# Kernel tuning notes

Hardware: AMD Instinct MI355X
Metric: run time of the kernel (lower is better)

The kernel has to match this reference:

```python
import jax, jax.numpy as jnp
import numpy as np

B, N, M = 1024, 65536, 128


def setup_inputs() -> dict:
    key = jax.random.key(0)
    k1, k2, k3, k4 = jax.random.split(key, 4)
    address = jax.random.uniform(k1, (B, N), dtype=jnp.float32)
    erase = jax.random.uniform(k2, (B, M), dtype=jnp.float32)
    add = jax.random.normal(k3, (B, M), dtype=jnp.float32)
    content = jax.random.uniform(k4, (N, M), dtype=jnp.float32)
    return {"address": address, "erase": erase, "add": add, "content": content}


def reference(address, erase, add, content):
    # write: outer-product erase/add aggregated over batch -> [N, M]
    erase_v = jnp.einsum('bn,bm->nm', address, erase)
    add_v = jnp.einsum('bn,bm->nm', address, add)
    new_content = content * (1.0 - erase_v) + add_v
    # read-after-write: [B,N] @ [N,M] -> [B,M]
    read_content = jnp.einsum('bn,nm->bm', address, new_content)
    return read_content
```

## Files before the change

kernel.cpp:

```cpp
#include <hip/hip_runtime.h>
#include <hip/hip_bf16.h>
#include <stdint.h>

#define B_SZ 1024
#define N_SZ 65536
#define M_SZ 128

typedef short bf16x8 __attribute__((ext_vector_type(8)));
typedef short bf16x4 __attribute__((ext_vector_type(4)));
typedef float f32x4 __attribute__((ext_vector_type(4)));

__device__ __forceinline__ unsigned short f2bf(float f) {
    uint32_t u = __float_as_uint(f);
    uint32_t r = (u + 0x7FFFu + ((u >> 16) & 1u)) >> 16;
    return (unsigned short)r;
}

__global__ __launch_bounds__(256) void k_edt(const float* __restrict__ E,
                                             const float* __restrict__ D,
                                             unsigned short* __restrict__ EDt) {
    __shared__ float tile[32][33];
    int bx = blockIdx.x & 31;
    int cy = blockIdx.x >> 5;
    int b0 = bx * 32, c0 = cy * 32;
    const float* src = (c0 < M_SZ) ? E : D;
    int cs0 = c0 & (M_SZ - 1);
    int t = threadIdx.x;
    int i = t >> 3, j = (t & 7) * 4;
    const float* p = src + (size_t)(b0 + i) * M_SZ + cs0 + j;
    float4 v = *(const float4*)p;
    tile[i][j] = v.x; tile[i][j + 1] = v.y; tile[i][j + 2] = v.z; tile[i][j + 3] = v.w;
    __syncthreads();
    int c = t >> 3, b4 = (t & 7) * 4;
    unsigned short* q = EDt + (size_t)(c0 + c) * B_SZ + b0 + b4;
    ushort4 o;
    o.x = f2bf(tile[b4 + 0][c]); o.y = f2bf(tile[b4 + 1][c]);
    o.z = f2bf(tile[b4 + 2][c]); o.w = f2bf(tile[b4 + 3][c]);
    *(ushort4*)q = o;
}

__global__ __launch_bounds__(256) void k_zero(float* __restrict__ out) {
    int i = blockIdx.x * 1024 + threadIdx.x * 4;
    *(float4*)(out + i) = (float4){0.f, 0.f, 0.f, 0.f};
}

#define AS_LD 132
#define ED_LD 40

__global__ __launch_bounds__(256, 2) void k_pass1(
    const float* __restrict__ A,
    const unsigned short* __restrict__ EDt,
    const float* __restrict__ C,
    unsigned short* __restrict__ NCt)
{
    __shared__ __align__(16) unsigned short As[2][32 * AS_LD];
    __shared__ __align__(16) unsigned short EDs[2][256 * ED_LD];
    const int t = threadIdx.x;
    const int lane = t & 63;
    const int wv = t >> 6;
    const int wvn = wv >> 1, wvc = wv & 1;
    const int g = lane >> 4;
    const int m16 = lane & 15;
    const int n0 = blockIdx.x * 128;

    const int kb = t >> 3;
    const int cA = (t & 7) * 16;
    const int colq = t >> 3;
    const int seg = t & 7;

    int cb[8];
#pragma unroll
    for (int fj = 0; fj < 4; ++fj) { cb[fj] = wvc * 4 + fj; cb[fj + 4] = 8 + wvc * 4 + fj; }

    f32x4 acc[4][8];
#pragma unroll
    for (int i = 0; i < 4; ++i)
#pragma unroll
        for (int j = 0; j < 8; ++j) acc[i][j] = (f32x4){0.f, 0.f, 0.f, 0.f};

    {
        const float* p = A + (size_t)kb * N_SZ + n0 + cA;
        float4 a0 = ((const float4*)p)[0], a1 = ((const float4*)p)[1];
        float4 a2 = ((const float4*)p)[2], a3 = ((const float4*)p)[3];
        ushort4* w = (ushort4*)&As[0][kb * AS_LD + cA];
        ushort4 o;
        o.x = f2bf(a0.x); o.y = f2bf(a0.y); o.z = f2bf(a0.z); o.w = f2bf(a0.w); w[0] = o;
        o.x = f2bf(a1.x); o.y = f2bf(a1.y); o.z = f2bf(a1.z); o.w = f2bf(a1.w); w[1] = o;
        o.x = f2bf(a2.x); o.y = f2bf(a2.y); o.z = f2bf(a2.z); o.w = f2bf(a2.w); w[2] = o;
        o.x = f2bf(a3.x); o.y = f2bf(a3.y); o.z = f2bf(a3.z); o.w = f2bf(a3.w); w[3] = o;
#pragma unroll
        for (int p8 = 0; p8 < 8; ++p8) {
            int col = p8 * 32 + colq;
            ushort4 v = *(const ushort4*)(EDt + (size_t)col * B_SZ + seg * 4);
            *(ushort4*)&EDs[0][col * ED_LD + seg * 4] = v;
        }
    }
    __syncthreads();

    int cur = 0;
    for (int bk = 0; bk < B_SZ; bk += 32) {
        const bool last = (bk + 32 >= B_SZ);
        const int nk = last ? 0 : bk + 32;

        const float* p = A + (size_t)(nk + kb) * N_SZ + n0 + cA;
        float4 a0 = ((const float4*)p)[0], a1 = ((const float4*)p)[1];
        float4 a2 = ((const float4*)p)[2], a3 = ((const float4*)p)[3];
        ushort4 e[8];
#pragma unroll
        for (int p8 = 0; p8 < 8; ++p8) {
            int col = p8 * 32 + colq;
            e[p8] = *(const ushort4*)(EDt + (size_t)col * B_SZ + nk + seg * 4);
        }

        bf16x8 af[4];
#pragma unroll
        for (int fi = 0; fi < 4; ++fi) {
            int nl = wvn * 64 + fi * 16 + m16;
#pragma unroll
            for (int j = 0; j < 8; ++j)
                af[fi][j] = (short)As[cur][(g * 8 + j) * AS_LD + nl];
        }
        bf16x8 bfr[8];
#pragma unroll
        for (int fj = 0; fj < 8; ++fj)
            bfr[fj] = *(const bf16x8*)&EDs[cur][(cb[fj] * 16 + m16) * ED_LD + g * 8];

#pragma unroll
        for (int fj = 0; fj < 8; ++fj)
#pragma unroll
            for (int fi = 0; fi < 4; ++fi)
                acc[fi][fj] = __builtin_amdgcn_mfma_f32_16x16x32_bf16(af[fi], bfr[fj], acc[fi][fj], 0, 0, 0);

        if (!last) {
            const int nxt = cur ^ 1;
            ushort4* w = (ushort4*)&As[nxt][kb * AS_LD + cA];
            ushort4 o;
            o.x = f2bf(a0.x); o.y = f2bf(a0.y); o.z = f2bf(a0.z); o.w = f2bf(a0.w); w[0] = o;
            o.x = f2bf(a1.x); o.y = f2bf(a1.y); o.z = f2bf(a1.z); o.w = f2bf(a1.w); w[1] = o;
            o.x = f2bf(a2.x); o.y = f2bf(a2.y); o.z = f2bf(a2.z); o.w = f2bf(a2.w); w[2] = o;
            o.x = f2bf(a3.x); o.y = f2bf(a3.y); o.z = f2bf(a3.z); o.w = f2bf(a3.w); w[3] = o;
#pragma unroll
            for (int p8 = 0; p8 < 8; ++p8) {
                int col = p8 * 32 + colq;
                *(ushort4*)&EDs[nxt][col * ED_LD + seg * 4] = e[p8];
            }
        }
        __syncthreads();
        cur ^= 1;
    }

#pragma unroll
    for (int fi = 0; fi < 4; ++fi)
#pragma unroll
        for (int fj = 0; fj < 4; ++fj) {
            int n_base = n0 + wvn * 64 + fi * 16 + g * 4;
            int m = wvc * 64 + fj * 16 + m16;
            bf16x4 o;
#pragma unroll
            for (int r = 0; r < 4; ++r) {
                float w = acc[fi][fj][r];
                float v = acc[fi][fj + 4][r];
                float cc = C[(size_t)(n_base + r) * M_SZ + m];
                o[r] = (short)f2bf(cc * (1.0f - w) + v);
            }
            *(bf16x4*)&NCt[(size_t)m * N_SZ + n_base] = o;
        }
}

#define L2_LD 40

__global__ __launch_bounds__(256, 2) void k_pass2(
    const float* __restrict__ A,
    const unsigned short* __restrict__ NCt,
    float* __restrict__ out)
{
    __shared__ __align__(16) unsigned short As2[2][128 * L2_LD];
    __shared__ __align__(16) unsigned short NCs[2][128 * L2_LD];
    const int t = threadIdx.x;
    const int lane = t & 63;
    const int wv = t >> 6;
    const int wvb = wv >> 1, wvm = wv & 1;
    const int g = lane >> 4;
    const int m16 = lane & 15;
    const int b0 = (blockIdx.x & 7) * 128;
    const int k0 = (blockIdx.x >> 3) * 1024;

    const int row = t >> 1, half = t & 1;

    f32x4 acc[4][4];
#pragma unroll
    for (int i = 0; i < 4; ++i)
#pragma unroll
        for (int j = 0; j < 4; ++j) acc[i][j] = (f32x4){0.f, 0.f, 0.f, 0.f};

    {
        const float* p = A + (size_t)(b0 + row) * N_SZ + k0 + half * 16;
        float4 a0 = ((const float4*)p)[0], a1 = ((const float4*)p)[1];
        float4 a2 = ((const float4*)p)[2], a3 = ((const float4*)p)[3];
        ushort4* w = (ushort4*)&As2[0][row * L2_LD + half * 16];
        ushort4 o;
        o.x = f2bf(a0.x); o.y = f2bf(a0.y); o.z = f2bf(a0.z); o.w = f2bf(a0.w); w[0] = o;
        o.x = f2bf(a1.x); o.y = f2bf(a1.y); o.z = f2bf(a1.z); o.w = f2bf(a1.w); w[1] = o;
        o.x = f2bf(a2.x); o.y = f2bf(a2.y); o.z = f2bf(a2.z); o.w = f2bf(a2.w); w[2] = o;
        o.x = f2bf(a3.x); o.y = f2bf(a3.y); o.z = f2bf(a3.z); o.w = f2bf(a3.w); w[3] = o;
        const uint4* pn = (const uint4*)(NCt + (size_t)row * N_SZ + k0 + half * 16);
        uint4 n0v = pn[0], n1v = pn[1];
        uint4* wn = (uint4*)&NCs[0][row * L2_LD + half * 16];
        wn[0] = n0v; wn[1] = n1v;
    }
    __syncthreads();

    int cur = 0;
    for (int kk = 0; kk < 1024; kk += 32) {
        const bool last = (kk + 32 >= 1024);
        const int nkk = last ? 0 : kk + 32;

        const float* p = A + (size_t)(b0 + row) * N_SZ + k0 + nkk + half * 16;
        float4 a0 = ((const float4*)p)[0], a1 = ((const float4*)p)[1];
        float4 a2 = ((const float4*)p)[2], a3 = ((const float4*)p)[3];
        const uint4* pn = (const uint4*)(NCt + (size_t)row * N_SZ + k0 + nkk + half * 16);
        uint4 n0v = pn[0], n1v = pn[1];

        bf16x8 af[4];
#pragma unroll
        for (int fi = 0; fi < 4; ++fi)
            af[fi] = *(const bf16x8*)&As2[cur][(wvb * 64 + fi * 16 + m16) * L2_LD + g * 8];
        bf16x8 bfr[4];
#pragma unroll
        for (int fj = 0; fj < 4; ++fj)
            bfr[fj] = *(const bf16x8*)&NCs[cur][(wvm * 64 + fj * 16 + m16) * L2_LD + g * 8];

#pragma unroll
        for (int fi = 0; fi < 4; ++fi)
#pragma unroll
            for (int fj = 0; fj < 4; ++fj)
                acc[fi][fj] = __builtin_amdgcn_mfma_f32_16x16x32_bf16(af[fi], bfr[fj], acc[fi][fj], 0, 0, 0);

        if (!last) {
            const int nxt = cur ^ 1;
            ushort4* w = (ushort4*)&As2[nxt][row * L2_LD + half * 16];
            ushort4 o;
            o.x = f2bf(a0.x); o.y = f2bf(a0.y); o.z = f2bf(a0.z); o.w = f2bf(a0.w); w[0] = o;
            o.x = f2bf(a1.x); o.y = f2bf(a1.y); o.z = f2bf(a1.z); o.w = f2bf(a1.w); w[1] = o;
            o.x = f2bf(a2.x); o.y = f2bf(a2.y); o.z = f2bf(a2.z); o.w = f2bf(a2.w); w[2] = o;
            o.x = f2bf(a3.x); o.y = f2bf(a3.y); o.z = f2bf(a3.z); o.w = f2bf(a3.w); w[3] = o;
            uint4* wn = (uint4*)&NCs[nxt][row * L2_LD + half * 16];
            wn[0] = n0v; wn[1] = n1v;
        }
        __syncthreads();
        cur ^= 1;
    }

#pragma unroll
    for (int fi = 0; fi < 4; ++fi)
#pragma unroll
        for (int fj = 0; fj < 4; ++fj)
#pragma unroll
            for (int r = 0; r < 4; ++r) {
                int b = b0 + wvb * 64 + fi * 16 + g * 4 + r;
                int m = wvm * 64 + fj * 16 + m16;
                atomicAdd(out + (size_t)b * M_SZ + m, acc[fi][fj][r]);
            }
}

extern "C" void kernel_launch(void* const* d_in, const int* in_sizes, int n_in,
                              void* d_out, int out_size, void* d_ws, size_t ws_size,
                              hipStream_t stream) {
    const float* A  = (const float*)d_in[0];
    const float* E  = (const float*)d_in[1];
    const float* Dd = (const float*)d_in[2];
    const float* C  = (const float*)d_in[3];
    float* out = (float*)d_out;

    unsigned short* NCt = (unsigned short*)d_ws;
    unsigned short* EDt = (unsigned short*)((char*)d_ws + (size_t)M_SZ * N_SZ * 2);

    k_edt <<<256, 256, 0, stream>>>(E, Dd, EDt);
    k_zero<<<128, 256, 0, stream>>>(out);
    k_pass1<<<512, 256, 0, stream>>>(A, EDt, C, NCt);
    k_pass2<<<512, 256, 0, stream>>>(A, NCt, out);
}
```

Before: 175.8 us.

## Drop LDS staging for pass2 and EDt operand, fuse zero into transpose

Pass2 now loads A and NCt fragments straight from global memory into registers in MFMA layout, with a two-stage register prefetch. This removes the LDS double buffers and barriers, and the block index mapping is swapped so consecutive blocks share a b-range. Pass1 reads the EDt B-operand directly from global (likely L2-resident) instead of staging it through LDS. The output zeroing is folded into the transpose kernel to save a launch. The risk is uncoalesced per-lane 32-byte global loads and more L2 traffic in exchange for fewer LDS round trips and syncs.

```diff
diff --git a/kernel.cpp b/kernel.cpp
--- a/kernel.cpp
+++ b/kernel.cpp
@@ -18,7 +18,13 @@
 
 __global__ __launch_bounds__(256) void k_edt(const float* __restrict__ E,
                                              const float* __restrict__ D,
-                                             unsigned short* __restrict__ EDt) {
+                                             unsigned short* __restrict__ EDt,
+                                             float* __restrict__ out) {
+    if (blockIdx.x >= 256) {
+        int i = (blockIdx.x - 256) * 1024 + threadIdx.x * 4;
+        *(float4*)(out + i) = (float4){0.f, 0.f, 0.f, 0.f};
+        return;
+    }
     __shared__ float tile[32][33];
     int bx = blockIdx.x & 31;
     int cy = blockIdx.x >> 5;
@@ -39,13 +45,7 @@
     *(ushort4*)q = o;
 }
 
-__global__ __launch_bounds__(256) void k_zero(float* __restrict__ out) {
-    int i = blockIdx.x * 1024 + threadIdx.x * 4;
-    *(float4*)(out + i) = (float4){0.f, 0.f, 0.f, 0.f};
-}
-
 #define AS_LD 132
-#define ED_LD 40
 
 __global__ __launch_bounds__(256, 2) void k_pass1(
     const float* __restrict__ A,
@@ -54,7 +54,6 @@
     unsigned short* __restrict__ NCt)
 {
     __shared__ __align__(16) unsigned short As[2][32 * AS_LD];
-    __shared__ __align__(16) unsigned short EDs[2][256 * ED_LD];
     const int t = threadIdx.x;
     const int lane = t & 63;
     const int wv = t >> 6;
@@ -65,12 +64,15 @@
 
     const int kb = t >> 3;
     const int cA = (t & 7) * 16;
-    const int colq = t >> 3;
-    const int seg = t & 7;
 
     int cb[8];
 #pragma unroll
     for (int fj = 0; fj < 4; ++fj) { cb[fj] = wvc * 4 + fj; cb[fj + 4] = 8 + wvc * 4 + fj; }
+
+    const unsigned short* edP[8];
+#pragma unroll
+    for (int fj = 0; fj < 8; ++fj)
+        edP[fj] = EDt + (size_t)(cb[fj] * 16 + m16) * B_SZ + g * 8;
 
     f32x4 acc[4][8];
 #pragma unroll
@@ -88,12 +90,6 @@
         o.x = f2bf(a1.x); o.y = f2bf(a1.y); o.z = f2bf(a1.z); o.w = f2bf(a1.w); w[1] = o;
         o.x = f2bf(a2.x); o.y = f2bf(a2.y); o.z = f2bf(a2.z); o.w = f2bf(a2.w); w[2] = o;
         o.x = f2bf(a3.x); o.y = f2bf(a3.y); o.z = f2bf(a3.z); o.w = f2bf(a3.w); w[3] = o;
-#pragma unroll
-        for (int p8 = 0; p8 < 8; ++p8) {
-            int col = p8 * 32 + colq;
-            ushort4 v = *(const ushort4*)(EDt + (size_t)col * B_SZ + seg * 4);
-            *(ushort4*)&EDs[0][col * ED_LD + seg * 4] = v;
-        }
     }
     __syncthreads();
 
@@ -105,12 +101,6 @@
         const float* p = A + (size_t)(nk + kb) * N_SZ + n0 + cA;
         float4 a0 = ((const float4*)p)[0], a1 = ((const float4*)p)[1];
         float4 a2 = ((const float4*)p)[2], a3 = ((const float4*)p)[3];
-        ushort4 e[8];
-#pragma unroll
-        for (int p8 = 0; p8 < 8; ++p8) {
-            int col = p8 * 32 + colq;
-            e[p8] = *(const ushort4*)(EDt + (size_t)col * B_SZ + nk + seg * 4);
-        }
 
         bf16x8 af[4];
 #pragma unroll
@@ -123,7 +113,7 @@
         bf16x8 bfr[8];
 #pragma unroll
         for (int fj = 0; fj < 8; ++fj)
-            bfr[fj] = *(const bf16x8*)&EDs[cur][(cb[fj] * 16 + m16) * ED_LD + g * 8];
+            bfr[fj] = *(const bf16x8*)(edP[fj] + bk);
 
 #pragma unroll
         for (int fj = 0; fj < 8; ++fj)
@@ -139,11 +129,6 @@
             o.x = f2bf(a1.x); o.y = f2bf(a1.y); o.z = f2bf(a1.z); o.w = f2bf(a1.w); w[1] = o;
             o.x = f2bf(a2.x); o.y = f2bf(a2.y); o.z = f2bf(a2.z); o.w = f2bf(a2.w); w[2] = o;
             o.x = f2bf(a3.x); o.y = f2bf(a3.y); o.z = f2bf(a3.z); o.w = f2bf(a3.w); w[3] = o;
-#pragma unroll
-            for (int p8 = 0; p8 < 8; ++p8) {
-                int col = p8 * 32 + colq;
-                *(ushort4*)&EDs[nxt][col * ED_LD + seg * 4] = e[p8];
-            }
         }
         __syncthreads();
         cur ^= 1;
@@ -167,25 +152,28 @@
         }
 }
 
-#define L2_LD 40
-
 __global__ __launch_bounds__(256, 2) void k_pass2(
     const float* __restrict__ A,
     const unsigned short* __restrict__ NCt,
     float* __restrict__ out)
 {
-    __shared__ __align__(16) unsigned short As2[2][128 * L2_LD];
-    __shared__ __align__(16) unsigned short NCs[2][128 * L2_LD];
     const int t = threadIdx.x;
     const int lane = t & 63;
     const int wv = t >> 6;
     const int wvb = wv >> 1, wvm = wv & 1;
     const int g = lane >> 4;
     const int m16 = lane & 15;
-    const int b0 = (blockIdx.x & 7) * 128;
-    const int k0 = (blockIdx.x >> 3) * 1024;
-
-    const int row = t >> 1, half = t & 1;
+    const int k0 = (blockIdx.x & 63) << 10;
+    const int b0 = (blockIdx.x >> 6) << 7;
+
+    const float* aP[4];
+    const unsigned short* nP[4];
+#pragma unroll
+    for (int fi = 0; fi < 4; ++fi)
+        aP[fi] = A + (size_t)(b0 + wvb * 64 + fi * 16 + m16) * N_SZ + k0 + g * 8;
+#pragma unroll
+    for (int fj = 0; fj < 4; ++fj)
+        nP[fj] = NCt + (size_t)(wvm * 64 + fj * 16 + m16) * N_SZ + k0 + g * 8;
 
     f32x4 acc[4][4];
 #pragma unroll
@@ -193,62 +181,49 @@
 #pragma unroll
         for (int j = 0; j < 4; ++j) acc[i][j] = (f32x4){0.f, 0.f, 0.f, 0.f};
 
-    {
-        const float* p = A + (size_t)(b0 + row) * N_SZ + k0 + half * 16;
-        float4 a0 = ((const float4*)p)[0], a1 = ((const float4*)p)[1];
-        float4 a2 = ((const float4*)p)[2], a3 = ((const float4*)p)[3];
-        ushort4* w = (ushort4*)&As2[0][row * L2_LD + half * 16];
-        ushort4 o;
-        o.x = f2bf(a0.x); o.y = f2bf(a0.y); o.z = f2bf(a0.z); o.w = f2bf(a0.w); w[0] = o;
-        o.x = f2bf(a1.x); o.y = f2bf(a1.y); o.z = f2bf(a1.z); o.w = f2bf(a1.w); w[1] = o;
-        o.x = f2bf(a2.x); o.y = f2bf(a2.y); o.z = f2bf(a2.z); o.w = f2bf(a2.w); w[2] = o;
-        o.x = f2bf(a3.x); o.y = f2bf(a3.y); o.z = f2bf(a3.z); o.w = f2bf(a3.w); w[3] = o;
-        const uint4* pn = (const uint4*)(NCt + (size_t)row * N_SZ + k0 + half * 16);
-        uint4 n0v = pn[0], n1v = pn[1];
-        uint4* wn = (uint4*)&NCs[0][row * L2_LD + half * 16];
-        wn[0] = n0v; wn[1] = n1v;
-    }
-    __syncthreads();
-
-    int cur = 0;
-    for (int kk = 0; kk < 1024; kk += 32) {
-        const bool last = (kk + 32 >= 1024);
-        const int nkk = last ? 0 : kk + 32;
-
-        const float* p = A + (size_t)(b0 + row) * N_SZ + k0 + nkk + half * 16;
-        float4 a0 = ((const float4*)p)[0], a1 = ((const float4*)p)[1];
-        float4 a2 = ((const float4*)p)[2], a3 = ((const float4*)p)[3];
-        const uint4* pn = (const uint4*)(NCt + (size_t)row * N_SZ + k0 + nkk + half * 16);
-        uint4 n0v = pn[0], n1v = pn[1];
-
+    float4 ra[2][4][2];
+    bf16x8 rb[2][4];
+
+#pragma unroll
+    for (int s = 0; s < 2; ++s) {
+#pragma unroll
+        for (int fi = 0; fi < 4; ++fi) {
+            ra[s][fi][0] = ((const float4*)(aP[fi] + s * 32))[0];
+            ra[s][fi][1] = ((const float4*)(aP[fi] + s * 32))[1];
+        }
+#pragma unroll
+        for (int fj = 0; fj < 4; ++fj)
+            rb[s][fj] = *(const bf16x8*)(nP[fj] + s * 32);
+    }
+
+#pragma unroll 2
+    for (int c = 0; c < 32; ++c) {
+        const int s = c & 1;
         bf16x8 af[4];
 #pragma unroll
+        for (int fi = 0; fi < 4; ++fi) {
+            af[fi][0] = (short)f2bf(ra[s][fi][0].x); af[fi][1] = (short)f2bf(ra[s][fi][0].y);
+            af[fi][2] = (short)f2bf(ra[s][fi][0].z); af[fi][3] = (short)f2bf(ra[s][fi][0].w);
+            af[fi][4] = (short)f2bf(ra[s][fi][1].x); af[fi][5] = (short)f2bf(ra[s][fi][1].y);
+            af[fi][6] = (short)f2bf(ra[s][fi][1].z); af[fi][7] = (short)f2bf(ra[s][fi][1].w);
+        }
+#pragma unroll
         for (int fi = 0; fi < 4; ++fi)
-            af[fi] = *(const bf16x8*)&As2[cur][(wvb * 64 + fi * 16 + m16) * L2_LD + g * 8];
-        bf16x8 bfr[4];
-#pragma unroll
-        for (int fj = 0; fj < 4; ++fj)
-            bfr[fj] = *(const bf16x8*)&NCs[cur][(wvm * 64 + fj * 16 + m16) * L2_LD + g * 8];
-
-#pragma unroll
-        for (int fi = 0; fi < 4; ++fi)
 #pragma unroll
             for (int fj = 0; fj < 4; ++fj)
-                acc[fi][fj] = __builtin_amdgcn_mfma_f32_16x16x32_bf16(af[fi], bfr[fj], acc[fi][fj], 0, 0, 0);
-
-        if (!last) {
-            const int nxt = cur ^ 1;
-            ushort4* w = (ushort4*)&As2[nxt][row * L2_LD + half * 16];
-            ushort4 o;
-            o.x = f2bf(a0.x); o.y = f2bf(a0.y); o.z = f2bf(a0.z); o.w = f2bf(a0.w); w[0] = o;
-            o.x = f2bf(a1.x); o.y = f2bf(a1.y); o.z = f2bf(a1.z); o.w = f2bf(a1.w); w[1] = o;
-            o.x = f2bf(a2.x); o.y = f2bf(a2.y); o.z = f2bf(a2.z); o.w = f2bf(a2.w); w[2] = o;
-            o.x = f2bf(a3.x); o.y = f2bf(a3.y); o.z = f2bf(a3.z); o.w = f2bf(a3.w); w[3] = o;
-            uint4* wn = (uint4*)&NCs[nxt][row * L2_LD + half * 16];
-            wn[0] = n0v; wn[1] = n1v;
-        }
-        __syncthreads();
-        cur ^= 1;
+                acc[fi][fj] = __builtin_amdgcn_mfma_f32_16x16x32_bf16(af[fi], rb[s][fj], acc[fi][fj], 0, 0, 0);
+
+        if (c + 2 < 32) {
+            const int off = (c + 2) * 32;
+#pragma unroll
+            for (int fi = 0; fi < 4; ++fi) {
+                ra[s][fi][0] = ((const float4*)(aP[fi] + off))[0];
+                ra[s][fi][1] = ((const float4*)(aP[fi] + off))[1];
+            }
+#pragma unroll
+            for (int fj = 0; fj < 4; ++fj)
+                rb[s][fj] = *(const bf16x8*)(nP[fj] + off);
+        }
     }
 
 #pragma unroll
@@ -275,8 +250,7 @@
     unsigned short* NCt = (unsigned short*)d_ws;
     unsigned short* EDt = (unsigned short*)((char*)d_ws + (size_t)M_SZ * N_SZ * 2);
 
-    k_edt <<<256, 256, 0, stream>>>(E, Dd, EDt);
-    k_zero<<<128, 256, 0, stream>>>(out);
+    k_edt <<<384, 256, 0, stream>>>(E, Dd, EDt, out);
     k_pass1<<<512, 256, 0, stream>>>(A, EDt, C, NCt);
     k_pass2<<<512, 256, 0, stream>>>(A, NCt, out);
 }
```

Result: slower. 223.3 us (+27.0%).
